# Optimization experiments

Hardware: AMD Instinct MI355X
Metric: run time of the kernel (lower is better)

Reference implementation:

```python
import jax, jax.numpy as jnp
import numpy as np
from jax import lax

EPS = 1e-6
CLAMP = 1e4


def _ln_last(x, w, b):
    # fp32 LayerNorm over last dim
    mu = jnp.mean(x, axis=-1, keepdims=True)
    var = jnp.mean(jnp.square(x - mu), axis=-1, keepdims=True)
    return (x - mu) * lax.rsqrt(var + EPS) * w + b


def _nan_clean(x):
    return jnp.nan_to_num(x, nan=0.0, posinf=CLAMP, neginf=-CLAMP)


def setup_inputs() -> dict:
    key = jax.random.key(0)
    B, C, H, W = 4, 256, 64, 64
    hid = 2 * C  # expand=2
    k = 3        # d_conv
    ks = jax.random.split(key, 12)
    s = 0.02
    return {
        "x": jax.random.normal(ks[0], (B, C, H, W), jnp.float32),
        "ln2d_w": jnp.ones((C,), jnp.float32),
        "ln2d_b": jnp.zeros((C,), jnp.float32),
        "inproj_w": jax.random.normal(ks[1], (C, C), jnp.float32) * s,
        "inproj_b": jnp.zeros((C,), jnp.float32),
        "dw2d_w": jax.random.normal(ks[2], (C, 3, 3), jnp.float32) * s,
        "dw2d_b": jnp.zeros((C,), jnp.float32),
        "ssm_ln_w": jnp.ones((C,), jnp.float32),
        "ssm_ln_b": jnp.zeros((C,), jnp.float32),
        "ssm_in_w": jax.random.normal(ks[3], (2 * hid, C), jnp.float32) * s,
        "ssm_in_b": jnp.zeros((2 * hid,), jnp.float32),
        "ssm_dw_w": jax.random.normal(ks[4], (hid, k), jnp.float32) * s,
        "ssm_dw_b": jnp.zeros((hid,), jnp.float32),
        "ssm_out_w": jax.random.normal(ks[5], (C, hid), jnp.float32) * s,
        "ssm_out_b": jnp.zeros((C,), jnp.float32),
        "outproj_w": jax.random.normal(ks[6], (C, C), jnp.float32) * s,
        "outproj_b": jnp.zeros((C,), jnp.float32),
    }


def reference(x, ln2d_w, ln2d_b, inproj_w, inproj_b, dw2d_w, dw2d_b,
              ssm_ln_w, ssm_ln_b, ssm_in_w, ssm_in_b, ssm_dw_w, ssm_dw_b,
              ssm_out_w, ssm_out_b, outproj_w, outproj_b):
    B, C, H, W = x.shape
    L = H * W

    # LN2d over channel dim (per-pixel LN on C)
    y = _ln_last(x.transpose(0, 2, 3, 1), ln2d_w, ln2d_b).transpose(0, 3, 1, 2)

    # 1x1 conv in_proj
    y = jnp.einsum('bchw,oc->bohw', y, inproj_w) + inproj_b[None, :, None, None]

    # depthwise 3x3 conv, SAME padding
    y = lax.conv_general_dilated(
        y, dw2d_w[:, None, :, :], (1, 1), ((1, 1), (1, 1)),
        dimension_numbers=('NCHW', 'OIHW', 'NCHW'),
        feature_group_count=C) + dw2d_b[None, :, None, None]

    # cross-scan: 4 routes (B,L,C)
    s0 = y.reshape(B, C, L).transpose(0, 2, 1)                      # row-major
    s1 = s0[:, ::-1]                                                # reversed
    s2 = y.transpose(0, 1, 3, 2).reshape(B, C, L).transpose(0, 2, 1)  # col-major
    s3 = s2[:, ::-1]
    s = jnp.concatenate([s0, s1, s2, s3], axis=0)  # (4B, L, C), shared SSM weights

    # MambaOrLite fallback: LN -> GLU -> depthwise conv1d -> out proj + residual
    r = _ln_last(s, ssm_ln_w, ssm_ln_b)
    r = r @ ssm_in_w.T + ssm_in_b                   # (4B, L, 2*hid)
    a, g = jnp.split(r, 2, axis=-1)
    r = a * jax.nn.sigmoid(g)                       # (4B, L, hid)
    r = r.transpose(0, 2, 1)                        # (4B, hid, L)
    hid = r.shape[1]
    k = ssm_dw_w.shape[-1]
    pad = ((k - 1) // 2, k // 2)
    r = lax.conv_general_dilated(
        r, ssm_dw_w[:, None, :], (1,), (pad,),
        dimension_numbers=('NCH', 'OIH', 'NCH'),
        feature_group_count=hid) + ssm_dw_b[None, :, None]
    r = r.transpose(0, 2, 1) @ ssm_out_w.T + ssm_out_b  # (4B, L, C)
    ys = _nan_clean(r) + s

    # cross-merge: average the 4 routes back to (B,C,H,W)
    y0, y1, y2, y3 = jnp.split(ys, 4, axis=0)
    m0 = y0.transpose(0, 2, 1).reshape(B, C, H, W)
    m1 = y1[:, ::-1].transpose(0, 2, 1).reshape(B, C, H, W)
    m2 = y2.transpose(0, 2, 1).reshape(B, C, W, H).transpose(0, 1, 3, 2)
    m3 = y3[:, ::-1].transpose(0, 2, 1).reshape(B, C, W, H).transpose(0, 1, 3, 2)
    m = (m0 + m1 + m2 + m3) * 0.25

    out = jnp.einsum('bchw,oc->bohw', m, outproj_w) + outproj_b[None, :, None, None]
    out = _nan_clean(out)
    return out + x
```

## Files before the change

### kernel.cpp

```cpp
#include <hip/hip_runtime.h>

typedef float f32x4 __attribute__((ext_vector_type(4)));
typedef __bf16 bf16x8 __attribute__((ext_vector_type(8)));
typedef unsigned short u16;
typedef unsigned int u32;

__device__ __forceinline__ float bf2f(u32 b) {
  u32 x = (b & 0xffffu) << 16;
  return __builtin_bit_cast(float, x);
}
__device__ __forceinline__ u16 f2bf(float f) {
  u32 x = __builtin_bit_cast(u32, f);
  x += 0x7fffu + ((x >> 16) & 1u);
  return (u16)(x >> 16);
}
__device__ __forceinline__ void gload16(const void* g, void* l) {
  __builtin_amdgcn_global_load_lds((__attribute__((address_space(1))) void*)g,
                                   (__attribute__((address_space(3))) void*)l,
                                   16, 0, 0);
}

__global__ __launch_bounds__(256)
void k_prep(const float* __restrict__ inproj_w, const float* __restrict__ ssm_in_w,
            const float* __restrict__ ssm_out_w, const float* __restrict__ outproj_w,
            const float* __restrict__ dw2d_w, const float* __restrict__ ssm_dw_w,
            const float* __restrict__ ssm_dw_b, const float* __restrict__ ssm_out_b,
            u16* __restrict__ w1b, u16* __restrict__ w2b, u16* __restrict__ w3b,
            u16* __restrict__ w4b, float* __restrict__ cvec, float* __restrict__ wT9,
            float* __restrict__ w02, float* __restrict__ w14) {
  int bid = blockIdx.x, tid = threadIdx.x;
  if (bid < 512) {
    const float* s; u16* d; int base;
    if (bid < 256)      { s = ssm_in_w;  d = w2b; base = bid; }
    else if (bid < 384) { s = ssm_out_w; d = w3b; base = bid - 256; }
    else if (bid < 448) { s = inproj_w;  d = w1b; base = bid - 384; }
    else                { s = outproj_w; d = w4b; base = bid - 448; }
    int i = base * 1024 + tid * 4;
    float4 v = *(const float4*)&s[i];
    u32 a = (u32)f2bf(v.x) | ((u32)f2bf(v.y) << 16);
    u32 b = (u32)f2bf(v.z) | ((u32)f2bf(v.w) << 16);
    *(uint2*)&d[i] = make_uint2(a, b);
  } else if (bid == 512) {
    float s = ssm_out_b[tid];
    const float* wr = ssm_out_w + (size_t)tid * 512;
    #pragma unroll 8
    for (int k = 0; k < 512; ++k) s += ssm_dw_b[k] * wr[k];
    cvec[tid] = s;
  } else {
    #pragma unroll
    for (int j = 0; j < 9; ++j) wT9[j * 256 + tid] = dw2d_w[tid * 9 + j];
    #pragma unroll
    for (int q = 0; q < 2; ++q) {
      int c = tid + q * 256;
      w02[c] = ssm_dw_w[c * 3 + 0] + ssm_dw_w[c * 3 + 2];
      w14[c] = 4.f * ssm_dw_w[c * 3 + 1];
    }
  }
}

__global__ __launch_bounds__(256, 2)
void k_ln2d(const float* __restrict__ x, const float* __restrict__ lw,
            const float* __restrict__ lb, u16* __restrict__ A) {
  __shared__ float T[256 * 65];
  __shared__ float ps1[4][64], ps2[4][64];
  __shared__ float mu[64], rsd[64];
  int tid = threadIdx.x, wv = tid >> 6, lane = tid & 63;
  int cq = lane >> 4, p4 = (lane & 15) * 4;
  int n0 = blockIdx.x * 64, bb = n0 >> 12, hw0 = n0 & 4095;
  const float* xb = x + ((size_t)bb << 20);
  float s0 = 0, s1 = 0, s2 = 0, s3 = 0;
  float q0 = 0, q1 = 0, q2 = 0, q3 = 0;
  #pragma unroll 4
  for (int i = 0; i < 16; ++i) {
    int c = wv * 64 + i * 4 + cq;
    float4 v = *(const float4*)&xb[((size_t)c << 12) + hw0 + p4];
    T[c * 65 + p4 + 0] = v.x; T[c * 65 + p4 + 1] = v.y;
    T[c * 65 + p4 + 2] = v.z; T[c * 65 + p4 + 3] = v.w;
    s0 += v.x; s1 += v.y; s2 += v.z; s3 += v.w;
    q0 += v.x * v.x; q1 += v.y * v.y; q2 += v.z * v.z; q3 += v.w * v.w;
  }
  #pragma unroll
  for (int off = 16; off < 64; off <<= 1) {
    s0 += __shfl_xor(s0, off); s1 += __shfl_xor(s1, off);
    s2 += __shfl_xor(s2, off); s3 += __shfl_xor(s3, off);
    q0 += __shfl_xor(q0, off); q1 += __shfl_xor(q1, off);
    q2 += __shfl_xor(q2, off); q3 += __shfl_xor(q3, off);
  }
  if (cq == 0) {
    ps1[wv][p4 + 0] = s0; ps1[wv][p4 + 1] = s1; ps1[wv][p4 + 2] = s2; ps1[wv][p4 + 3] = s3;
    ps2[wv][p4 + 0] = q0; ps2[wv][p4 + 1] = q1; ps2[wv][p4 + 2] = q2; ps2[wv][p4 + 3] = q3;
  }
  __syncthreads();
  if (tid < 64) {
    float S1 = ps1[0][tid] + ps1[1][tid] + ps1[2][tid] + ps1[3][tid];
    float S2 = ps2[0][tid] + ps2[1][tid] + ps2[2][tid] + ps2[3][tid];
    float m = S1 * (1.f / 256.f);
    float var = S2 * (1.f / 256.f) - m * m;
    mu[tid] = m;
    rsd[tid] = rsqrtf(var + 1e-6f);
  }
  __syncthreads();
  int c4b = (tid & 15) * 4, p2b = tid >> 4;
  #pragma unroll
  for (int cc = 0; cc < 4; ++cc) {
    int c4 = cc * 64 + c4b;
    float4 w4 = *(const float4*)&lw[c4];
    float4 g4 = *(const float4*)&lb[c4];
    #pragma unroll
    for (int i2 = 0; i2 < 4; ++i2) {
      int p2 = p2b + 16 * i2;
      float m = mu[p2], rs = rsd[p2];
      float o0 = (T[(c4 + 0) * 65 + p2] - m) * rs * w4.x + g4.x;
      float o1 = (T[(c4 + 1) * 65 + p2] - m) * rs * w4.y + g4.y;
      float o2 = (T[(c4 + 2) * 65 + p2] - m) * rs * w4.z + g4.z;
      float o3 = (T[(c4 + 3) * 65 + p2] - m) * rs * w4.w + g4.w;
      u32 a = (u32)f2bf(o0) | ((u32)f2bf(o1) << 16);
      u32 b = (u32)f2bf(o2) | ((u32)f2bf(o3) << 16);
      *(uint2*)&A[(size_t)(n0 + p2) * 256 + c4] = make_uint2(a, b);
    }
  }
}

__global__ __launch_bounds__(256)
void k_dw3x3_ln(const u16* __restrict__ Y1, const float* __restrict__ wT,
                const float* __restrict__ dwb, const float* __restrict__ lnw,
                const float* __restrict__ lnb, u16* __restrict__ Yc,
                u16* __restrict__ A) {
  int tid = threadIdx.x;
  int n = blockIdx.x * 4 + (tid >> 6);
  int lane = tid & 63;
  int c0 = lane * 4;
  int b = n >> 12, hw = n & 4095, h = hw >> 6, w = hw & 63;
  float4 b4 = *(const float4*)&dwb[c0];
  float a0 = b4.x, a1 = b4.y, a2 = b4.z, a3 = b4.w;
  #pragma unroll
  for (int ky = 0; ky < 3; ++ky) {
    int hh = h + ky - 1;
    if (hh < 0 || hh > 63) continue;
    #pragma unroll
    for (int kx = 0; kx < 3; ++kx) {
      int ww = w + kx - 1;
      if (ww < 0 || ww > 63) continue;
      size_t nn = ((size_t)b << 12) + (hh << 6) + ww;
      uint2 u = *(const uint2*)&Y1[nn * 256 + c0];
      float4 w4 = *(const float4*)&wT[(ky * 3 + kx) * 256 + c0];
      a0 += bf2f(u.x) * w4.x;
      a1 += bf2f(u.x >> 16) * w4.y;
      a2 += bf2f(u.y) * w4.z;
      a3 += bf2f(u.y >> 16) * w4.w;
    }
  }
  u32 p0 = (u32)f2bf(a0) | ((u32)f2bf(a1) << 16);
  u32 p1 = (u32)f2bf(a2) | ((u32)f2bf(a3) << 16);
  *(uint2*)&Yc[(size_t)n * 256 + c0] = make_uint2(p0, p1);
  float s1 = a0 + a1 + a2 + a3;
  float s2 = a0 * a0 + a1 * a1 + a2 * a2 + a3 * a3;
  #pragma unroll
  for (int off = 1; off < 64; off <<= 1) {
    s1 += __shfl_xor(s1, off);
    s2 += __shfl_xor(s2, off);
  }
  float m = s1 * (1.f / 256.f);
  float var = s2 * (1.f / 256.f) - m * m;
  float rs = rsqrtf(var + 1e-6f);
  float4 w4 = *(const float4*)&lnw[c0];
  float4 g4 = *(const float4*)&lnb[c0];
  float o0 = (a0 - m) * rs * w4.x + g4.x;
  float o1 = (a1 - m) * rs * w4.y + g4.y;
  float o2 = (a2 - m) * rs * w4.z + g4.z;
  float o3 = (a3 - m) * rs * w4.w + g4.w;
  u32 qa = (u32)f2bf(o0) | ((u32)f2bf(o1) << 16);
  u32 qb = (u32)f2bf(o2) | ((u32)f2bf(o3) << 16);
  *(uint2*)&A[(size_t)n * 256 + c0] = make_uint2(qa, qb);
}

__global__ __launch_bounds__(256)
void k_scan(const u16* __restrict__ G, const float* __restrict__ w02,
            const float* __restrict__ w14, u16* __restrict__ Z) {
  int tid = threadIdx.x;
  int n = blockIdx.x * 2 + (tid >> 7);
  int c0 = (tid & 127) * 4;
  int b = n >> 12, hw = n & 4095, h = hw >> 6, w = hw & 63;
  int m = w * 64 + h;
  float s0 = 0.f, s1 = 0.f, s2 = 0.f, s3 = 0.f;
  auto addn = [&](int nn) {
    uint2 u = *(const uint2*)&G[(size_t)nn * 512 + c0];
    s0 += bf2f(u.x); s1 += bf2f(u.x >> 16);
    s2 += bf2f(u.y); s3 += bf2f(u.y >> 16);
  };
  if (hw > 0) addn(n - 1);
  if (hw < 4095) addn(n + 1);
  if (m > 0)    { int mm = m - 1; addn((b << 12) + ((mm & 63) << 6) + (mm >> 6)); }
  if (m < 4095) { int mm = m + 1; addn((b << 12) + ((mm & 63) << 6) + (mm >> 6)); }
  uint2 uc = *(const uint2*)&G[(size_t)n * 512 + c0];
  float g0 = bf2f(uc.x), g1 = bf2f(uc.x >> 16), g2 = bf2f(uc.y), g3 = bf2f(uc.y >> 16);
  float4 wa = *(const float4*)&w02[c0];
  float4 wb = *(const float4*)&w14[c0];
  float z0 = wa.x * s0 + wb.x * g0;
  float z1 = wa.y * s1 + wb.y * g1;
  float z2 = wa.z * s2 + wb.z * g2;
  float z3 = wa.w * s3 + wb.w * g3;
  u32 p0 = (u32)f2bf(z0) | ((u32)f2bf(z1) << 16);
  u32 p1 = (u32)f2bf(z2) | ((u32)f2bf(z3) << 16);
  *(uint2*)&Z[(size_t)n * 512 + c0] = make_uint2(p0, p1);
}

template <int EPI>
__global__ __launch_bounds__(256, 4)
void k_gemm2(const u16* __restrict__ R, const u16* __restrict__ Cm,
             const float* __restrict__ bias, int K, int nCt, int ldo,
             u16* __restrict__ outb, const u16* __restrict__ resb,
             float* __restrict__ outf, const float* __restrict__ resf) {
  __shared__ u16 tR[2][64 * 32];
  __shared__ u16 tC[2][128 * 32];
  int tid = threadIdx.x, lane = tid & 63, wv = tid >> 6;
  int rt = blockIdx.x / nCt, ct = blockIdx.x % nCt;
  int r0 = rt * 64, c0 = ct * 128;
  int fr = lane & 15, kc = lane >> 4;
  int sr = lane >> 2, sc = (lane & 3) * 8;
  f32x4 acc[4][2] = {};
  int nK = K >> 5;
  const u16* gR  = R  + (size_t)(r0 + wv * 16 + sr) * K + sc;
  const u16* gC0 = Cm + (size_t)(c0 + wv * 32 + sr) * K + sc;
  const u16* gC1 = Cm + (size_t)(c0 + wv * 32 + 16 + sr) * K + sc;
  auto STAGE = [&](int buf, int kt) {
    int k0 = kt * 32;
    gload16(gR + k0,  &tR[buf][wv * 16 * 32]);
    gload16(gC0 + k0, &tC[buf][(wv * 32) * 32]);
    gload16(gC1 + k0, &tC[buf][(wv * 32 + 16) * 32]);
  };
  auto COMPUTE = [&](int buf) {
    bf16x8 af[4], wf[2];
    #pragma unroll
    for (int m = 0; m < 4; ++m)
      af[m] = *(const bf16x8*)&tR[buf][(m * 16 + fr) * 32 + kc * 8];
    #pragma unroll
    for (int n = 0; n < 2; ++n)
      wf[n] = *(const bf16x8*)&tC[buf][(wv * 32 + n * 16 + fr) * 32 + kc * 8];
    #pragma unroll
    for (int m = 0; m < 4; ++m)
      #pragma unroll
      for (int n = 0; n < 2; ++n)
        acc[m][n] = __builtin_amdgcn_mfma_f32_16x16x32_bf16(af[m], wf[n], acc[m][n], 0, 0, 0);
  };
  STAGE(0, 0);
  __syncthreads();
  int cur = 0;
  for (int kt = 0; kt < nK - 1; ++kt) {
    STAGE(cur ^ 1, kt + 1);
    __builtin_amdgcn_sched_barrier(0);
    COMPUTE(cur);
    __syncthreads();
    cur ^= 1;
  }
  COMPUTE(cur);
  #pragma unroll
  for (int m = 0; m < 4; ++m) {
    #pragma unroll
    for (int n = 0; n < 2; ++n) {
      #pragma unroll
      for (int r = 0; r < 4; ++r) {
        float v = acc[m][n][r];
        if (EPI == 0) {
          int gn = r0 + m * 16 + kc * 4 + r;
          int go = c0 + wv * 32 + n * 16 + fr;
          outb[(size_t)gn * ldo + go] = f2bf(v + bias[go]);
        } else if (EPI == 1) {
          int gn = r0 + m * 16 + kc * 4 + r;
          int go = c0 + wv * 32 + n * 16 + fr;
          outb[(size_t)gn * 256 + go] =
              f2bf(0.25f * v + bias[go] + bf2f(resb[(size_t)gn * 256 + go]));
        } else {
          int go = r0 + m * 16 + kc * 4 + r;
          int gn = c0 + wv * 32 + n * 16 + fr;
          int b = gn >> 12, hw = gn & 4095;
          size_t idx = (((size_t)(b * 256 + go)) << 12) + hw;
          outf[idx] = v + bias[go] + resf[idx];
        }
      }
    }
  }
}

__global__ __launch_bounds__(256, 3)
void k_gate2(const u16* __restrict__ A, const u16* __restrict__ W,
             const float* __restrict__ bias, u16* __restrict__ G) {
  __shared__ u16 tR[2][64 * 32];
  __shared__ u16 tCa[2][128 * 32];
  __shared__ u16 tCg[2][128 * 32];
  int tid = threadIdx.x, lane = tid & 63, wv = tid >> 6;
  int rt = blockIdx.x >> 2, ot = blockIdx.x & 3;
  int r0 = rt * 64, o0 = ot * 128;
  int fr = lane & 15, kc = lane >> 4;
  int sr = lane >> 2, sc = (lane & 3) * 8;
  const int K = 256;
  f32x4 acca[4][2] = {}, accg[4][2] = {};
  const u16* gR  = A + (size_t)(r0 + wv * 16 + sr) * K + sc;
  const u16* gA0 = W + (size_t)(o0 + wv * 32 + sr) * K + sc;
  const u16* gA1 = W + (size_t)(o0 + wv * 32 + 16 + sr) * K + sc;
  const u16* gG0 = W + (size_t)(512 + o0 + wv * 32 + sr) * K + sc;
  const u16* gG1 = W + (size_t)(512 + o0 + wv * 32 + 16 + sr) * K + sc;
  auto STAGE = [&](int buf, int kt) {
    int k0 = kt * 32;
    gload16(gR + k0,  &tR[buf][wv * 16 * 32]);
    gload16(gA0 + k0, &tCa[buf][(wv * 32) * 32]);
    gload16(gA1 + k0, &tCa[buf][(wv * 32 + 16) * 32]);
    gload16(gG0 + k0, &tCg[buf][(wv * 32) * 32]);
    gload16(gG1 + k0, &tCg[buf][(wv * 32 + 16) * 32]);
  };
  auto COMPUTE = [&](int buf) {
    bf16x8 af[4], wa[2], wg[2];
    #pragma unroll
    for (int m = 0; m < 4; ++m)
      af[m] = *(const bf16x8*)&tR[buf][(m * 16 + fr) * 32 + kc * 8];
    #pragma unroll
    for (int n = 0; n < 2; ++n) {
      wa[n] = *(const bf16x8*)&tCa[buf][(wv * 32 + n * 16 + fr) * 32 + kc * 8];
      wg[n] = *(const bf16x8*)&tCg[buf][(wv * 32 + n * 16 + fr) * 32 + kc * 8];
    }
    #pragma unroll
    for (int m = 0; m < 4; ++m)
      #pragma unroll
      for (int n = 0; n < 2; ++n) {
        acca[m][n] = __builtin_amdgcn_mfma_f32_16x16x32_bf16(af[m], wa[n], acca[m][n], 0, 0, 0);
        accg[m][n] = __builtin_amdgcn_mfma_f32_16x16x32_bf16(af[m], wg[n], accg[m][n], 0, 0, 0);
      }
  };
  STAGE(0, 0);
  __syncthreads();
  int cur = 0;
  for (int kt = 0; kt < 7; ++kt) {
    STAGE(cur ^ 1, kt + 1);
    __builtin_amdgcn_sched_barrier(0);
    COMPUTE(cur);
    __syncthreads();
    cur ^= 1;
  }
  COMPUTE(cur);
  #pragma unroll
  for (int m = 0; m < 4; ++m) {
    #pragma unroll
    for (int n = 0; n < 2; ++n) {
      #pragma unroll
      for (int r = 0; r < 4; ++r) {
        int gn = r0 + m * 16 + kc * 4 + r;
        int go = o0 + wv * 32 + n * 16 + fr;
        float a = acca[m][n][r] + bias[go];
        float g = accg[m][n][r] + bias[512 + go];
        G[(size_t)gn * 512 + go] = f2bf(a / (1.f + expf(-g)));
      }
    }
  }
}

extern "C" void kernel_launch(void* const* d_in, const int* in_sizes, int n_in,
                              void* d_out, int out_size, void* d_ws, size_t ws_size,
                              hipStream_t stream) {
  const float* x         = (const float*)d_in[0];
  const float* ln2d_w    = (const float*)d_in[1];
  const float* ln2d_b    = (const float*)d_in[2];
  const float* inproj_w  = (const float*)d_in[3];
  const float* inproj_b  = (const float*)d_in[4];
  const float* dw2d_w    = (const float*)d_in[5];
  const float* dw2d_b    = (const float*)d_in[6];
  const float* ssm_ln_w  = (const float*)d_in[7];
  const float* ssm_ln_b  = (const float*)d_in[8];
  const float* ssm_in_w  = (const float*)d_in[9];
  const float* ssm_in_b  = (const float*)d_in[10];
  const float* ssm_dw_w  = (const float*)d_in[11];
  const float* ssm_dw_b  = (const float*)d_in[12];
  const float* ssm_out_w = (const float*)d_in[13];
  const float* ssm_out_b = (const float*)d_in[14];
  const float* outproj_w = (const float*)d_in[15];
  const float* outproj_b = (const float*)d_in[16];
  float* out = (float*)d_out;

  char* ws = (char*)d_ws;
  size_t off = 0;
  auto take = [&](size_t bytes) -> char* {
    char* p = ws + off;
    off = (off + bytes + 255) & ~(size_t)255;
    return p;
  };
  u16* w1b    = (u16*)take(65536 * 2);
  u16* w2b    = (u16*)take(262144 * 2);
  u16* w3b    = (u16*)take(131072 * 2);
  u16* w4b    = (u16*)take(65536 * 2);
  float* cvec = (float*)take(256 * 4);
  float* wT9  = (float*)take(9 * 256 * 4);
  float* w02  = (float*)take(512 * 4);
  float* w14  = (float*)take(512 * 4);
  u16* Abuf   = (u16*)take((size_t)16384 * 256 * 2);
  u16* Y1     = (u16*)take((size_t)16384 * 256 * 2);
  u16* Yc     = (u16*)take((size_t)16384 * 256 * 2);
  u16* G      = (u16*)take((size_t)16384 * 512 * 2);
  u16* Z      = (u16*)take((size_t)16384 * 512 * 2);
  (void)ws_size; (void)in_sizes; (void)n_in; (void)out_size;

  k_prep<<<514, 256, 0, stream>>>(inproj_w, ssm_in_w, ssm_out_w, outproj_w,
                                  dw2d_w, ssm_dw_w, ssm_dw_b, ssm_out_b,
                                  w1b, w2b, w3b, w4b, cvec, wT9, w02, w14);
  k_ln2d<<<256, 256, 0, stream>>>(x, ln2d_w, ln2d_b, Abuf);
  k_gemm2<0><<<512, 256, 0, stream>>>(Abuf, w1b, inproj_b, 256, 2, 256,
                                      Y1, nullptr, nullptr, nullptr);
  k_dw3x3_ln<<<4096, 256, 0, stream>>>(Y1, wT9, dw2d_b, ssm_ln_w, ssm_ln_b, Yc, Abuf);
  k_gate2<<<1024, 256, 0, stream>>>(Abuf, w2b, ssm_in_b, G);
  k_scan<<<8192, 256, 0, stream>>>(G, w02, w14, Z);
  k_gemm2<1><<<512, 256, 0, stream>>>(Z, w3b, cvec, 512, 2, 256,
                                      Abuf, Yc, nullptr, nullptr);
  k_gemm2<2><<<512, 256, 0, stream>>>(w4b, Abuf, outproj_b, 256, 128, 0,
                                      nullptr, nullptr, out, x);
}
```

Baseline: 113.0 us.

## Fuse scan stencil into ssm_out GEMM and merge weight prep into LN kernel

```diff
diff --git a/kernel.cpp b/kernel.cpp
--- a/kernel.cpp
+++ b/kernel.cpp
@@ -20,53 +20,54 @@
                                    16, 0, 0);
 }
 
-__global__ __launch_bounds__(256)
-void k_prep(const float* __restrict__ inproj_w, const float* __restrict__ ssm_in_w,
-            const float* __restrict__ ssm_out_w, const float* __restrict__ outproj_w,
-            const float* __restrict__ dw2d_w, const float* __restrict__ ssm_dw_w,
-            const float* __restrict__ ssm_dw_b, const float* __restrict__ ssm_out_b,
-            u16* __restrict__ w1b, u16* __restrict__ w2b, u16* __restrict__ w3b,
-            u16* __restrict__ w4b, float* __restrict__ cvec, float* __restrict__ wT9,
-            float* __restrict__ w02, float* __restrict__ w14) {
-  int bid = blockIdx.x, tid = threadIdx.x;
-  if (bid < 512) {
-    const float* s; u16* d; int base;
-    if (bid < 256)      { s = ssm_in_w;  d = w2b; base = bid; }
-    else if (bid < 384) { s = ssm_out_w; d = w3b; base = bid - 256; }
-    else if (bid < 448) { s = inproj_w;  d = w1b; base = bid - 384; }
-    else                { s = outproj_w; d = w4b; base = bid - 448; }
-    int i = base * 1024 + tid * 4;
-    float4 v = *(const float4*)&s[i];
-    u32 a = (u32)f2bf(v.x) | ((u32)f2bf(v.y) << 16);
-    u32 b = (u32)f2bf(v.z) | ((u32)f2bf(v.w) << 16);
-    *(uint2*)&d[i] = make_uint2(a, b);
-  } else if (bid == 512) {
-    float s = ssm_out_b[tid];
-    const float* wr = ssm_out_w + (size_t)tid * 512;
-    #pragma unroll 8
-    for (int k = 0; k < 512; ++k) s += ssm_dw_b[k] * wr[k];
-    cvec[tid] = s;
-  } else {
-    #pragma unroll
-    for (int j = 0; j < 9; ++j) wT9[j * 256 + tid] = dw2d_w[tid * 9 + j];
-    #pragma unroll
-    for (int q = 0; q < 2; ++q) {
-      int c = tid + q * 256;
-      w02[c] = ssm_dw_w[c * 3 + 0] + ssm_dw_w[c * 3 + 2];
-      w14[c] = 4.f * ssm_dw_w[c * 3 + 1];
-    }
-  }
-}
-
 __global__ __launch_bounds__(256, 2)
-void k_ln2d(const float* __restrict__ x, const float* __restrict__ lw,
-            const float* __restrict__ lb, u16* __restrict__ A) {
+void k_ln2d_prep(const float* __restrict__ x, const float* __restrict__ lw,
+                 const float* __restrict__ lb, u16* __restrict__ A,
+                 const float* __restrict__ inproj_w, const float* __restrict__ ssm_in_w,
+                 const float* __restrict__ ssm_out_w, const float* __restrict__ outproj_w,
+                 const float* __restrict__ dw2d_w, const float* __restrict__ ssm_dw_w,
+                 const float* __restrict__ ssm_dw_b, const float* __restrict__ ssm_out_b,
+                 u16* __restrict__ w1b, u16* __restrict__ w2b, u16* __restrict__ w3b,
+                 u16* __restrict__ w4b, float* __restrict__ cvec, float* __restrict__ wT9,
+                 float* __restrict__ w02, float* __restrict__ w14) {
   __shared__ float T[256 * 65];
   __shared__ float ps1[4][64], ps2[4][64];
   __shared__ float mu[64], rsd[64];
-  int tid = threadIdx.x, wv = tid >> 6, lane = tid & 63;
+  int bid = blockIdx.x, tid = threadIdx.x;
+  if (bid >= 256) {
+    int pb = bid - 256;
+    if (pb < 512) {
+      const float* s; u16* d; int base;
+      if (pb < 256)      { s = ssm_in_w;  d = w2b; base = pb; }
+      else if (pb < 384) { s = ssm_out_w; d = w3b; base = pb - 256; }
+      else if (pb < 448) { s = inproj_w;  d = w1b; base = pb - 384; }
+      else               { s = outproj_w; d = w4b; base = pb - 448; }
+      int i = base * 1024 + tid * 4;
+      float4 v = *(const float4*)&s[i];
+      u32 a = (u32)f2bf(v.x) | ((u32)f2bf(v.y) << 16);
+      u32 b = (u32)f2bf(v.z) | ((u32)f2bf(v.w) << 16);
+      *(uint2*)&d[i] = make_uint2(a, b);
+    } else if (pb == 512) {
+      float s = ssm_out_b[tid];
+      const float* wr = ssm_out_w + (size_t)tid * 512;
+      #pragma unroll 8
+      for (int k = 0; k < 512; ++k) s += ssm_dw_b[k] * wr[k];
+      cvec[tid] = s;
+    } else {
+      #pragma unroll
+      for (int j = 0; j < 9; ++j) wT9[j * 256 + tid] = dw2d_w[tid * 9 + j];
+      #pragma unroll
+      for (int q = 0; q < 2; ++q) {
+        int c = tid + q * 256;
+        w02[c] = ssm_dw_w[c * 3 + 0] + ssm_dw_w[c * 3 + 2];
+        w14[c] = 4.f * ssm_dw_w[c * 3 + 1];
+      }
+    }
+    return;
+  }
+  int wv = tid >> 6, lane = tid & 63;
   int cq = lane >> 4, p4 = (lane & 15) * 4;
-  int n0 = blockIdx.x * 64, bb = n0 >> 12, hw0 = n0 & 4095;
+  int n0 = bid * 64, bb = n0 >> 12, hw0 = n0 & 4095;
   const float* xb = x + ((size_t)bb << 20);
   float s0 = 0, s1 = 0, s2 = 0, s3 = 0;
   float q0 = 0, q1 = 0, q2 = 0, q3 = 0;
@@ -174,43 +175,12 @@
   *(uint2*)&A[(size_t)n * 256 + c0] = make_uint2(qa, qb);
 }
 
-__global__ __launch_bounds__(256)
-void k_scan(const u16* __restrict__ G, const float* __restrict__ w02,
-            const float* __restrict__ w14, u16* __restrict__ Z) {
-  int tid = threadIdx.x;
-  int n = blockIdx.x * 2 + (tid >> 7);
-  int c0 = (tid & 127) * 4;
-  int b = n >> 12, hw = n & 4095, h = hw >> 6, w = hw & 63;
-  int m = w * 64 + h;
-  float s0 = 0.f, s1 = 0.f, s2 = 0.f, s3 = 0.f;
-  auto addn = [&](int nn) {
-    uint2 u = *(const uint2*)&G[(size_t)nn * 512 + c0];
-    s0 += bf2f(u.x); s1 += bf2f(u.x >> 16);
-    s2 += bf2f(u.y); s3 += bf2f(u.y >> 16);
-  };
-  if (hw > 0) addn(n - 1);
-  if (hw < 4095) addn(n + 1);
-  if (m > 0)    { int mm = m - 1; addn((b << 12) + ((mm & 63) << 6) + (mm >> 6)); }
-  if (m < 4095) { int mm = m + 1; addn((b << 12) + ((mm & 63) << 6) + (mm >> 6)); }
-  uint2 uc = *(const uint2*)&G[(size_t)n * 512 + c0];
-  float g0 = bf2f(uc.x), g1 = bf2f(uc.x >> 16), g2 = bf2f(uc.y), g3 = bf2f(uc.y >> 16);
-  float4 wa = *(const float4*)&w02[c0];
-  float4 wb = *(const float4*)&w14[c0];
-  float z0 = wa.x * s0 + wb.x * g0;
-  float z1 = wa.y * s1 + wb.y * g1;
-  float z2 = wa.z * s2 + wb.z * g2;
-  float z3 = wa.w * s3 + wb.w * g3;
-  u32 p0 = (u32)f2bf(z0) | ((u32)f2bf(z1) << 16);
-  u32 p1 = (u32)f2bf(z2) | ((u32)f2bf(z3) << 16);
-  *(uint2*)&Z[(size_t)n * 512 + c0] = make_uint2(p0, p1);
-}
-
 template <int EPI>
 __global__ __launch_bounds__(256, 4)
 void k_gemm2(const u16* __restrict__ R, const u16* __restrict__ Cm,
              const float* __restrict__ bias, int K, int nCt, int ldo,
-             u16* __restrict__ outb, const u16* __restrict__ resb,
-             float* __restrict__ outf, const float* __restrict__ resf) {
+             u16* __restrict__ outb, float* __restrict__ outf,
+             const float* __restrict__ resf) {
   __shared__ u16 tR[2][64 * 32];
   __shared__ u16 tC[2][128 * 32];
   int tid = threadIdx.x, lane = tid & 63, wv = tid >> 6;
@@ -265,11 +235,6 @@
           int gn = r0 + m * 16 + kc * 4 + r;
           int go = c0 + wv * 32 + n * 16 + fr;
           outb[(size_t)gn * ldo + go] = f2bf(v + bias[go]);
-        } else if (EPI == 1) {
-          int gn = r0 + m * 16 + kc * 4 + r;
-          int go = c0 + wv * 32 + n * 16 + fr;
-          outb[(size_t)gn * 256 + go] =
-              f2bf(0.25f * v + bias[go] + bf2f(resb[(size_t)gn * 256 + go]));
         } else {
           int go = r0 + m * 16 + kc * 4 + r;
           int gn = c0 + wv * 32 + n * 16 + fr;
@@ -353,6 +318,108 @@
   }
 }
 
+__global__ __launch_bounds__(256, 2)
+void k_gemm_scan(const u16* __restrict__ G, const u16* __restrict__ W3,
+                 const float* __restrict__ w02, const float* __restrict__ w14,
+                 const float* __restrict__ cvec, const u16* __restrict__ Yc,
+                 u16* __restrict__ M) {
+  __shared__ u16 tR[2][32 * 32];
+  __shared__ u16 tC[2][256 * 32];
+  int tid = threadIdx.x, lane = tid & 63, wv = tid >> 6;
+  int r0 = blockIdx.x * 32;
+  int fr = lane & 15, kc = lane >> 4;
+  int zrow = tid >> 3;
+  int zg = (tid & 7) * 4;
+  int n = r0 + zrow;
+  int b = n >> 12, hw = n & 4095, h = hw >> 6, w = hw & 63;
+  int m = w * 64 + h;
+  int mm1 = m - 1, mp1 = m + 1;
+  size_t o_c = (size_t)n * 512 + zg;
+  size_t o_p = (size_t)(hw > 0 ? n - 1 : n) * 512 + zg;
+  size_t o_n = (size_t)(hw < 4095 ? n + 1 : n) * 512 + zg;
+  size_t o_u = (size_t)(m > 0 ? ((b << 12) + ((mm1 & 63) << 6) + (mm1 >> 6)) : n) * 512 + zg;
+  size_t o_d = (size_t)(m < 4095 ? ((b << 12) + ((mp1 & 63) << 6) + (mp1 >> 6)) : n) * 512 + zg;
+  float mP = hw > 0 ? 1.f : 0.f, mN = hw < 4095 ? 1.f : 0.f;
+  float mU = m > 0 ? 1.f : 0.f, mD = m < 4095 ? 1.f : 0.f;
+  f32x4 acc[2][4] = {};
+  auto STAGE_C = [&](int buf, int kt) {
+    int k0 = kt * 32;
+    #pragma unroll
+    for (int i = 0; i < 4; ++i) {
+      int s0 = wv * 256 + i * 64;
+      int s = s0 + lane;
+      int row = s >> 2, off = (s & 3) * 8;
+      gload16(W3 + (size_t)row * 512 + k0 + off, &tC[buf][s0 * 8]);
+    }
+  };
+  uint2 lc, lp, ln_, lu, ld;
+  float4 va, vb;
+  auto ZLOAD = [&](int kt) {
+    int c = kt * 32 + zg;
+    lc = *(const uint2*)&G[o_c + (kt * 32)];
+    lp = *(const uint2*)&G[o_p + (kt * 32)];
+    ln_ = *(const uint2*)&G[o_n + (kt * 32)];
+    lu = *(const uint2*)&G[o_u + (kt * 32)];
+    ld = *(const uint2*)&G[o_d + (kt * 32)];
+    va = *(const float4*)&w02[c];
+    vb = *(const float4*)&w14[c];
+  };
+  auto ZSTORE = [&](int buf) {
+    float s_0 = mP * bf2f(lp.x) + mN * bf2f(ln_.x) + mU * bf2f(lu.x) + mD * bf2f(ld.x);
+    float s_1 = mP * bf2f(lp.x >> 16) + mN * bf2f(ln_.x >> 16) + mU * bf2f(lu.x >> 16) + mD * bf2f(ld.x >> 16);
+    float s_2 = mP * bf2f(lp.y) + mN * bf2f(ln_.y) + mU * bf2f(lu.y) + mD * bf2f(ld.y);
+    float s_3 = mP * bf2f(lp.y >> 16) + mN * bf2f(ln_.y >> 16) + mU * bf2f(lu.y >> 16) + mD * bf2f(ld.y >> 16);
+    float z0 = va.x * s_0 + vb.x * bf2f(lc.x);
+    float z1 = va.y * s_1 + vb.y * bf2f(lc.x >> 16);
+    float z2 = va.z * s_2 + vb.z * bf2f(lc.y);
+    float z3 = va.w * s_3 + vb.w * bf2f(lc.y >> 16);
+    u32 p0 = (u32)f2bf(z0) | ((u32)f2bf(z1) << 16);
+    u32 p1 = (u32)f2bf(z2) | ((u32)f2bf(z3) << 16);
+    *(uint2*)&tR[buf][zrow * 32 + zg] = make_uint2(p0, p1);
+  };
+  auto COMPUTE = [&](int buf) {
+    bf16x8 af[2], wf[4];
+    #pragma unroll
+    for (int mi = 0; mi < 2; ++mi)
+      af[mi] = *(const bf16x8*)&tR[buf][(mi * 16 + fr) * 32 + kc * 8];
+    #pragma unroll
+    for (int ni = 0; ni < 4; ++ni)
+      wf[ni] = *(const bf16x8*)&tC[buf][(wv * 64 + ni * 16 + fr) * 32 + kc * 8];
+    #pragma unroll
+    for (int mi = 0; mi < 2; ++mi)
+      #pragma unroll
+      for (int ni = 0; ni < 4; ++ni)
+        acc[mi][ni] = __builtin_amdgcn_mfma_f32_16x16x32_bf16(af[mi], wf[ni], acc[mi][ni], 0, 0, 0);
+  };
+  STAGE_C(0, 0);
+  ZLOAD(0);
+  ZSTORE(0);
+  __syncthreads();
+  int cur = 0;
+  for (int kt = 0; kt < 15; ++kt) {
+    ZLOAD(kt + 1);
+    STAGE_C(cur ^ 1, kt + 1);
+    COMPUTE(cur);
+    ZSTORE(cur ^ 1);
+    __syncthreads();
+    cur ^= 1;
+  }
+  COMPUTE(cur);
+  #pragma unroll
+  for (int mi = 0; mi < 2; ++mi) {
+    #pragma unroll
+    for (int ni = 0; ni < 4; ++ni) {
+      #pragma unroll
+      for (int r = 0; r < 4; ++r) {
+        int gn = r0 + mi * 16 + kc * 4 + r;
+        int go = wv * 64 + ni * 16 + fr;
+        size_t idx = (size_t)gn * 256 + go;
+        M[idx] = f2bf(0.25f * acc[mi][ni][r] + cvec[go] + bf2f(Yc[idx]));
+      }
+    }
+  }
+}
+
 extern "C" void kernel_launch(void* const* d_in, const int* in_sizes, int n_in,
                               void* d_out, int out_size, void* d_ws, size_t ws_size,
                               hipStream_t stream) {
@@ -394,20 +461,17 @@
   u16* Y1     = (u16*)take((size_t)16384 * 256 * 2);
   u16* Yc     = (u16*)take((size_t)16384 * 256 * 2);
   u16* G      = (u16*)take((size_t)16384 * 512 * 2);
-  u16* Z      = (u16*)take((size_t)16384 * 512 * 2);
   (void)ws_size; (void)in_sizes; (void)n_in; (void)out_size;
 
-  k_prep<<<514, 256, 0, stream>>>(inproj_w, ssm_in_w, ssm_out_w, outproj_w,
-                                  dw2d_w, ssm_dw_w, ssm_dw_b, ssm_out_b,
-                                  w1b, w2b, w3b, w4b, cvec, wT9, w02, w14);
-  k_ln2d<<<256, 256, 0, stream>>>(x, ln2d_w, ln2d_b, Abuf);
+  k_ln2d_prep<<<770, 256, 0, stream>>>(x, ln2d_w, ln2d_b, Abuf,
+                                       inproj_w, ssm_in_w, ssm_out_w, outproj_w,
+                                       dw2d_w, ssm_dw_w, ssm_dw_b, ssm_out_b,
+                                       w1b, w2b, w3b, w4b, cvec, wT9, w02, w14);
   k_gemm2<0><<<512, 256, 0, stream>>>(Abuf, w1b, inproj_b, 256, 2, 256,
-                                      Y1, nullptr, nullptr, nullptr);
+                                      Y1, nullptr, nullptr);
   k_dw3x3_ln<<<4096, 256, 0, stream>>>(Y1, wT9, dw2d_b, ssm_ln_w, ssm_ln_b, Yc, Abuf);
   k_gate2<<<1024, 256, 0, stream>>>(Abuf, w2b, ssm_in_b, G);
-  k_scan<<<8192, 256, 0, stream>>>(G, w02, w14, Z);
-  k_gemm2<1><<<512, 256, 0, stream>>>(Z, w3b, cvec, 512, 2, 256,
-                                      Abuf, Yc, nullptr, nullptr);
+  k_gemm_scan<<<512, 256, 0, stream>>>(G, w3b, w02, w14, cvec, Yc, Abuf);
   k_gemm2<2><<<512, 256, 0, stream>>>(w4b, Abuf, outproj_b, 256, 128, 0,
-                                      nullptr, nullptr, out, x);
-}
+                                      nullptr, out, x);
+}
```

Result: faster. 105.7 us (-6.5%).
